# Performance work log

Measured on AMD Instinct MI355X. Metric: run time of the kernel, lower is better.

The kernel has to match this reference:

```python
import jax, jax.numpy as jnp
import numpy as np
import math

B, S, D, H = 4, 1024, 1024, 16
DH = D // H  # 64
NEG = -100000000000.0


def setup_inputs() -> dict:
    key = jax.random.key(0)
    ks = jax.random.split(key, 9)
    sc_in = 1.0 / math.sqrt(D)
    sc_h = 1.0 / math.sqrt(DH)
    return {
        "x": jax.random.normal(ks[0], (B, S, D), dtype=jnp.float32),
        # per-head projection weights stacked over the head axis [H, D, DH]
        "Wq": jax.random.normal(ks[1], (H, D, DH), dtype=jnp.float32) * sc_in,
        "bq": jnp.zeros((H, DH), dtype=jnp.float32),
        "Wk": jax.random.normal(ks[2], (H, D, DH), dtype=jnp.float32) * sc_in,
        "bk": jnp.zeros((H, DH), dtype=jnp.float32),
        "Wv": jax.random.normal(ks[3], (H, D, DH), dtype=jnp.float32) * sc_in,
        "bv": jnp.zeros((H, DH), dtype=jnp.float32),
        # output feed-forward: Dense(D, gelu) applied to the [B,S,DH] head-sum
        "Wf": jax.random.normal(ks[4], (DH, D), dtype=jnp.float32) * sc_h,
        "bf": jnp.zeros((D,), dtype=jnp.float32),
    }


def reference(x, Wq, bq, Wk, bk, Wv, bv, Wf, bf):
    # per-head q,k,v: [B,H,S,DH]
    q = jnp.einsum('bsd,hde->bhse', x, Wq) + bq[None, :, None, :]
    k = jnp.einsum('bsd,hde->bhse', x, Wk) + bk[None, :, None, :]
    v = jnp.einsum('bsd,hde->bhse', x, Wv) + bv[None, :, None, :]
    scale = 1.0 / math.sqrt(DH)
    # causal mask as in source: triu(ones, 1) * -1e11 added to scores
    mask = jnp.triu(jnp.ones((S, S), dtype=jnp.float32), 1) * NEG
    scores = jnp.einsum('bhse,bhte->bhst', q, k) * scale + mask  # [B,H,S,S]
    w = jax.nn.softmax(scores, axis=-1)
    z = jnp.einsum('bhst,bhte->bhse', w, v)  # [B,H,S,DH]
    # faithful to source bug: heads are SUMMED, not concatenated
    summed = jnp.sum(z, axis=1)  # [B,S,DH]
    # ff Dense with exact (erf) gelu, keras tf.nn.gelu default approximate=False
    out = jax.nn.gelu(summed @ Wf + bf, approximate=False)  # [B,S,D]
    # dropout is identity at inference
    return out
```

## Files before the change

### kernel.cpp

```cpp
#include <hip/hip_runtime.h>
#include <hip/hip_bf16.h>
#include <math.h>

#define BB 4
#define SS 1024
#define DD 1024
#define HH 16
#define DH 64

#define GM 4096
#define GN 3072
#define GK 1024

typedef __attribute__((ext_vector_type(4))) float f32x4;
typedef __attribute__((ext_vector_type(8))) short bf16x8;

__device__ __forceinline__ unsigned int pack2bf(float a, float b) {
    __hip_bfloat16 x = __float2bfloat16(a), y = __float2bfloat16(b);
    return (unsigned int)__builtin_bit_cast(unsigned short, x) |
           ((unsigned int)__builtin_bit_cast(unsigned short, y) << 16);
}

__device__ __forceinline__ int swz8(int row) { return (row ^ (row >> 2)) & 7; }

__global__ __launch_bounds__(256) void prep_kernel(
    const float* __restrict__ x, __hip_bfloat16* __restrict__ xb,
    const float* __restrict__ Wq, const float* __restrict__ Wk,
    const float* __restrict__ Wv, __hip_bfloat16* __restrict__ WbT,
    const float* __restrict__ Wf, unsigned short* __restrict__ WfT)
{
    const int id  = blockIdx.x;
    const int tid = threadIdx.x;
    __shared__ float tile[64][65];

    if (id < 4096) {
        int i = (id * 256 + tid) * 4;
        float4 xv = *(const float4*)(x + i);
        xb[i + 0] = __float2bfloat16(xv.x);
        xb[i + 1] = __float2bfloat16(xv.y);
        xb[i + 2] = __float2bfloat16(xv.z);
        xb[i + 3] = __float2bfloat16(xv.w);
    } else if (id < 4864) {
        const int idx = id - 4096;
        const int d0  = (idx & 15) * 64;
        const int zh  = idx >> 4;
        const int z   = zh >> 4;
        const int h   = zh & 15;
        const float* W = (z == 0) ? Wq : (z == 1) ? Wk : Wv;
        const float* src = W + (size_t)h * DD * DH;
        #pragma unroll
        for (int p = 0; p < 16; p++) {
            int d = p * 4 + (tid >> 6);
            int e = tid & 63;
            tile[d][e] = src[(size_t)(d0 + d) * DH + e];
        }
        __syncthreads();
        #pragma unroll
        for (int p = 0; p < 16; p++) {
            int e = p * 4 + (tid >> 6);
            int d = tid & 63;
            WbT[(size_t)(z * 1024 + h * 64 + e) * GK + d0 + d] =
                __float2bfloat16(tile[d][e]);
        }
    } else {
        const int d0 = (id - 4864) * 64;
        #pragma unroll
        for (int p = 0; p < 16; p++) {
            int e  = p * 4 + (tid >> 6);
            int dd = tid & 63;
            tile[e][dd] = Wf[(size_t)e * DD + d0 + dd];
        }
        __syncthreads();
        #pragma unroll
        for (int p = 0; p < 16; p++) {
            int dd = p * 4 + (tid >> 6);
            int e  = tid & 63;
            __hip_bfloat16 hb = __float2bfloat16(tile[e][dd]);
            WfT[(size_t)(d0 + dd) * DH + e] =
                __builtin_bit_cast(unsigned short, hb);
        }
    }
}

__global__ __launch_bounds__(256) void gemm_qkv(
    const unsigned short* __restrict__ A,
    const unsigned short* __restrict__ Bt,
    const float* __restrict__ bq, const float* __restrict__ bk,
    const float* __restrict__ bv,
    unsigned short* __restrict__ q, unsigned short* __restrict__ k,
    unsigned short* __restrict__ v)
{
    __shared__ unsigned short As[2][128 * 32];
    __shared__ unsigned short Bs[2][128 * 32];

    const int tid  = threadIdx.x;
    const int wave = tid >> 6;
    const int lane = tid & 63;
    const int m0 = blockIdx.x * 128;
    const int n0 = blockIdx.y * 128;
    const int wy = wave >> 1, wx = wave & 1;
    const bool vblk = (n0 >= 2048);

    f32x4 acc[4][4];
    #pragma unroll
    for (int i = 0; i < 4; i++)
        #pragma unroll
        for (int j = 0; j < 4; j++)
            acc[i][j] = (f32x4){0.f, 0.f, 0.f, 0.f};

    const int lrow2 = lane >> 2;
    const int lslot = lane & 3;
    const int kchsw = lslot ^ ((lrow2 >> 1) & 3);

    #define STAGE(bufidx, ki)                                                  \
        {                                                                      \
            int k0 = (ki) * 32;                                                \
            _Pragma("unroll")                                                  \
            for (int c = 0; c < 2; c++) {                                      \
                int region = wave * 2 + c;                                     \
                int row = region * 16 + lrow2;                                 \
                const unsigned short* ga =                                     \
                    A + (size_t)(m0 + row) * GK + k0 + kchsw * 8;              \
                const unsigned short* gb =                                     \
                    Bt + (size_t)(n0 + row) * GK + k0 + kchsw * 8;             \
                __builtin_amdgcn_global_load_lds(                              \
                    (const __attribute__((address_space(1))) unsigned int*)ga, \
                    (__attribute__((address_space(3))) unsigned int*)          \
                        (&As[bufidx][region * 512]), 16, 0, 0);                \
                __builtin_amdgcn_global_load_lds(                              \
                    (const __attribute__((address_space(1))) unsigned int*)gb, \
                    (__attribute__((address_space(3))) unsigned int*)          \
                        (&Bs[bufidx][region * 512]), 16, 0, 0);                \
            }                                                                  \
        }

    STAGE(0, 0);

    const int mrow = lane & 15;
    const int quad = lane >> 4;

    for (int ki = 0; ki < 32; ki++) {
        __syncthreads();
        if (ki < 31) STAGE((ki + 1) & 1, ki + 1);

        const unsigned short* uA = &As[ki & 1][0];
        const unsigned short* uB = &Bs[ki & 1][0];

        bf16x8 af[4], bfr[4];
        #pragma unroll
        for (int mt = 0; mt < 4; mt++) {
            int row = wy * 64 + mt * 16 + mrow;
            int chunk = quad ^ ((row >> 1) & 3);
            af[mt] = *(const bf16x8*)(uA + row * 32 + chunk * 8);
        }
        #pragma unroll
        for (int nt = 0; nt < 4; nt++) {
            int row = wx * 64 + nt * 16 + mrow;
            int chunk = quad ^ ((row >> 1) & 3);
            bfr[nt] = *(const bf16x8*)(uB + row * 32 + chunk * 8);
        }
        if (vblk) {
            #pragma unroll
            for (int mt = 0; mt < 4; mt++)
                #pragma unroll
                for (int nt = 0; nt < 4; nt++)
                    acc[mt][nt] = __builtin_amdgcn_mfma_f32_16x16x32_bf16(
                        af[mt], bfr[nt], acc[mt][nt], 0, 0, 0);
        } else {
            #pragma unroll
            for (int nt = 0; nt < 4; nt++)
                #pragma unroll
                for (int mt = 0; mt < 4; mt++)
                    acc[nt][mt] = __builtin_amdgcn_mfma_f32_16x16x32_bf16(
                        bfr[nt], af[mt], acc[nt][mt], 0, 0, 0);
        }
    }
    #undef STAGE

    const int cl = lane & 15;
    const int h  = ((n0 + wx * 64) >> 6) & 15;

    if (!vblk) {
        const int z = n0 >> 10;
        const float* bias = (z == 0) ? bq : bk;
        unsigned short* outp = (z == 0) ? q : k;
        const float sc = (z == 0) ? 0.125f : 1.0f;
        #pragma unroll
        for (int nt = 0; nt < 4; nt++) {
            int ebase = nt * 16 + quad * 4;
            float4 b4 = *(const float4*)(bias + h * 64 + ebase);
            #pragma unroll
            for (int mt = 0; mt < 4; mt++) {
                int m = m0 + wy * 64 + mt * 16 + cl;
                int b = m >> 10, s = m & 1023;
                f32x4 a = acc[nt][mt];
                float v0 = (a[0] + b4.x) * sc;
                float v1 = (a[1] + b4.y) * sc;
                float v2 = (a[2] + b4.z) * sc;
                float v3 = (a[3] + b4.w) * sc;
                uint2 pk = make_uint2(pack2bf(v0, v1), pack2bf(v2, v3));
                *(uint2*)(outp + ((size_t)((b * 16 + h) * 1024 + s)) * 64 + ebase) = pk;
            }
        }
    } else {
        #pragma unroll
        for (int nt = 0; nt < 4; nt++) {
            int e = nt * 16 + cl;
            float bb = bv[h * 64 + e];
            #pragma unroll
            for (int mt = 0; mt < 4; mt++) {
                int rbase = m0 + wy * 64 + mt * 16 + quad * 4;
                int b = rbase >> 10, s = rbase & 1023;
                f32x4 a = acc[mt][nt];
                uint2 pk = make_uint2(pack2bf(a[0] + bb, a[1] + bb),
                                      pack2bf(a[2] + bb, a[3] + bb));
                *(uint2*)(v + ((size_t)((b * 16 + h) * 64 + e)) * 1024 + s) = pk;
            }
        }
    }
}

__global__ __launch_bounds__(256) void flash_attn(
    const unsigned short* __restrict__ qg, const unsigned short* __restrict__ kg,
    const unsigned short* __restrict__ vtg, float* __restrict__ summed)
{
    __shared__ unsigned short Qs[4096];
    __shared__ unsigned short Ks[2][4096];
    __shared__ unsigned short Vts[2][4096];

    const int x  = blockIdx.x;
    const int y  = blockIdx.y;
    const int qi = (x + (y & 15) + ((y >> 4) << 2)) & 15;
    const int q0 = qi * 64;
    const int bh = y;
    const int b  = bh >> 4;
    const int tid  = threadIdx.x;
    const int wave = tid >> 6;
    const int lane = tid & 63;
    const int lrow = lane >> 3;
    const int lcs  = lane & 7;
    const int m16  = lane & 15;
    const int quad = lane >> 4;

    const unsigned short* qb = qg + (size_t)bh * SS * DH;
    const unsigned short* kb = kg + (size_t)bh * SS * DH;
    const unsigned short* vb = vtg + (size_t)bh * SS * DH;

    #pragma unroll
    for (int c = 0; c < 2; c++) {
        int region = wave * 2 + c;
        int row = region * 8 + lrow;
        int g = lcs ^ swz8(row);
        __builtin_amdgcn_global_load_lds(
            (const __attribute__((address_space(1))) unsigned int*)
                (qb + (size_t)(q0 + row) * DH + g * 8),
            (__attribute__((address_space(3))) unsigned int*)(Qs + region * 512),
            16, 0, 0);
        __builtin_amdgcn_global_load_lds(
            (const __attribute__((address_space(1))) unsigned int*)
                (kb + (size_t)row * DH + g * 8),
            (__attribute__((address_space(3))) unsigned int*)(&Ks[0][region * 512]),
            16, 0, 0);
        __builtin_amdgcn_global_load_lds(
            (const __attribute__((address_space(1))) unsigned int*)
                (vb + (size_t)row * SS + g * 8),
            (__attribute__((address_space(3))) unsigned int*)(&Vts[0][region * 512]),
            16, 0, 0);
    }

    f32x4 accO[4];
    float lsum = 0.f;
    #pragma unroll
    for (int nt = 0; nt < 4; nt++) accO[nt] = (f32x4){0.f, 0.f, 0.f, 0.f};

    bf16x8 af0, af1;
    const int rloc = wave * 16 + m16;

    for (int tt = 0; tt <= qi; tt++) {
        __syncthreads();

        if (tt == 0) {
            int row = wave * 16 + m16;
            af0 = *(const bf16x8*)(Qs + row * 64 + ((quad ^ swz8(row)) * 8));
            af1 = *(const bf16x8*)(Qs + row * 64 + (((4 + quad) ^ swz8(row)) * 8));
        }

        if (tt < qi) {
            const int t1 = (tt + 1) * 64;
            const int bn = (tt + 1) & 1;
            #pragma unroll
            for (int c = 0; c < 2; c++) {
                int region = wave * 2 + c;
                int row = region * 8 + lrow;
                int g = lcs ^ swz8(row);
                __builtin_amdgcn_global_load_lds(
                    (const __attribute__((address_space(1))) unsigned int*)
                        (kb + (size_t)(t1 + row) * DH + g * 8),
                    (__attribute__((address_space(3))) unsigned int*)
                        (&Ks[bn][region * 512]), 16, 0, 0);
                __builtin_amdgcn_global_load_lds(
                    (const __attribute__((address_space(1))) unsigned int*)
                        (vb + (size_t)row * SS + t1 + g * 8),
                    (__attribute__((address_space(3))) unsigned int*)
                        (&Vts[bn][region * 512]), 16, 0, 0);
            }
        }

        const unsigned short* uK = &Ks[tt & 1][0];
        const unsigned short* uV = &Vts[tt & 1][0];

        f32x4 acc[4];
        #pragma unroll
        for (int nt = 0; nt < 4; nt++) {
            int row = ((nt & 2) << 4) + ((m16 >> 2) << 3) + ((nt & 1) << 2) + (m16 & 3);
            bf16x8 kf0 = *(const bf16x8*)(uK + row * 64 + ((quad ^ swz8(row)) * 8));
            bf16x8 kf1 = *(const bf16x8*)(uK + row * 64 + (((4 + quad) ^ swz8(row)) * 8));
            f32x4 a = (f32x4){0.f, 0.f, 0.f, 0.f};
            a = __builtin_amdgcn_mfma_f32_16x16x32_bf16(kf0, af0, a, 0, 0, 0);
            a = __builtin_amdgcn_mfma_f32_16x16x32_bf16(kf1, af1, a, 0, 0, 0);
            acc[nt] = a;
        }

        const bool diag = (tt == qi);
        bf16x8 pf0, pf1;
        #pragma unroll
        for (int nt = 0; nt < 4; nt++) {
            #pragma unroll
            for (int r = 0; r < 4; r++) {
                int tl = ((nt & 2) << 4) + (quad << 3) + ((nt & 1) << 2) + r;
                float s = acc[nt][r];
                if (diag && tl > rloc) s = -1e30f;
                float p = __expf(s);
                lsum += p;
                __hip_bfloat16 hb = __float2bfloat16(p);
                short pb = (short)__builtin_bit_cast(unsigned short, hb);
                int j = ((nt & 1) << 2) + r;
                if (nt < 2) pf0[j] = pb; else pf1[j] = pb;
            }
        }

        #pragma unroll
        for (int nt = 0; nt < 4; nt++) {
            int row = nt * 16 + m16;
            bf16x8 vf0 = *(const bf16x8*)(uV + row * 64 + ((quad ^ swz8(row)) * 8));
            bf16x8 vf1 = *(const bf16x8*)(uV + row * 64 + (((4 + quad) ^ swz8(row)) * 8));
            accO[nt] = __builtin_amdgcn_mfma_f32_16x16x32_bf16(vf0, pf0, accO[nt],
                                                               0, 0, 0);
            accO[nt] = __builtin_amdgcn_mfma_f32_16x16x32_bf16(vf1, pf1, accO[nt],
                                                               0, 0, 0);
        }
    }

    float l = lsum;
    l += __shfl_xor(l, 16);
    l += __shfl_xor(l, 32);
    const float invl = 1.f / l;

    __syncthreads();
    float* buf = (wave < 2) ? (float*)&Ks[0][0] : (float*)&Vts[0][0];
    buf += (wave & 1) * (16 * 66);
    #pragma unroll
    for (int nt = 0; nt < 4; nt++) {
        f32x4 w4 = accO[nt];
        w4 *= invl;
        *(f32x4*)(buf + m16 * 66 + nt * 16 + quad * 4) = w4;
    }
    __asm__ volatile("s_waitcnt lgkmcnt(0)" ::: "memory");

    float* dstbase = summed + ((size_t)b * SS + q0 + wave * 16) * DH;
    #pragma unroll
    for (int rr = 0; rr < 16; rr++) {
        float valr = buf[rr * 66 + lane];
        atomicAdd(dstbase + (size_t)rr * DH + lane, valr);
    }
}

__global__ __launch_bounds__(256) void ff_mfma(
    const float* __restrict__ summed, const unsigned short* __restrict__ WfT,
    const float* __restrict__ bfb, float* __restrict__ out)
{
    __shared__ unsigned short As[128 * 64];
    __shared__ unsigned short Bs[128 * 64];

    const int tid  = threadIdx.x;
    const int wave = tid >> 6;
    const int lane = tid & 63;
    const int m0 = blockIdx.x * 128;
    const int n0 = blockIdx.y * 128;
    const int wy = wave >> 1, wx = wave & 1;
    const int lrow = lane >> 3;
    const int lcs  = lane & 7;

    #pragma unroll
    for (int c = 0; c < 4; c++) {
        int row = (wave * 4 + c) * 8 + lrow;
        int chunk = lcs ^ (row & 7);
        __builtin_amdgcn_global_load_lds(
            (const __attribute__((address_space(1))) unsigned int*)
                (WfT + (size_t)(n0 + row) * DH + chunk * 8),
            (__attribute__((address_space(3))) unsigned int*)
                (Bs + ((wave * 4 + c) * 64) * 8), 16, 0, 0);
    }
    #pragma unroll
    for (int i = 0; i < 4; i++) {
        int chunkid = tid + i * 256;
        int row = chunkid >> 3, c = chunkid & 7;
        const float* src = summed + (size_t)(m0 + row) * DH + c * 8;
        float4 a = *(const float4*)src;
        float4 bq = *(const float4*)(src + 4);
        uint4 pk;
        pk.x = pack2bf(a.x, a.y);  pk.y = pack2bf(a.z, a.w);
        pk.z = pack2bf(bq.x, bq.y); pk.w = pack2bf(bq.z, bq.w);
        *(uint4*)(As + row * 64 + ((c ^ (row & 7)) * 8)) = pk;
    }
    __syncthreads();

    f32x4 acc[4][4];
    #pragma unroll
    for (int i = 0; i < 4; i++)
        #pragma unroll
        for (int j = 0; j < 4; j++)
            acc[i][j] = (f32x4){0.f, 0.f, 0.f, 0.f};

    const int mrow = lane & 15;
    const int quad = lane >> 4;
    #pragma unroll
    for (int ks = 0; ks < 2; ks++) {
        bf16x8 af[4], bfr[4];
        #pragma unroll
        for (int mt = 0; mt < 4; mt++) {
            int row = wy * 64 + mt * 16 + mrow;
            int chunk = (ks * 4 + quad) ^ (row & 7);
            af[mt] = *(const bf16x8*)(As + row * 64 + chunk * 8);
        }
        #pragma unroll
        for (int nt = 0; nt < 4; nt++) {
            int row = wx * 64 + nt * 16 + mrow;
            int chunk = (ks * 4 + quad) ^ (row & 7);
            bfr[nt] = *(const bf16x8*)(Bs + row * 64 + chunk * 8);
        }
        #pragma unroll
        for (int mt = 0; mt < 4; mt++)
            #pragma unroll
            for (int nt = 0; nt < 4; nt++)
                acc[mt][nt] = __builtin_amdgcn_mfma_f32_16x16x32_bf16(
                    af[mt], bfr[nt], acc[mt][nt], 0, 0, 0);
    }

    const int cl = lane & 15;
    #pragma unroll
    for (int nt = 0; nt < 4; nt++) {
        int d = n0 + wx * 64 + nt * 16 + cl;
        float bb = bfb[d];
        #pragma unroll
        for (int mt = 0; mt < 4; mt++) {
            int rbase = m0 + wy * 64 + mt * 16 + quad * 4;
            #pragma unroll
            for (int r = 0; r < 4; r++) {
                float vA = acc[mt][nt][r] + bb;
                out[(size_t)(rbase + r) * DD + d] =
                    0.5f * vA * (1.f + erff(vA * 0.70710678118654752f));
            }
        }
    }
}

extern "C" void kernel_launch(void* const* d_in, const int* in_sizes, int n_in,
                              void* d_out, int out_size, void* d_ws, size_t ws_size,
                              hipStream_t stream) {
    const float* x  = (const float*)d_in[0];
    const float* Wq = (const float*)d_in[1];
    const float* bq = (const float*)d_in[2];
    const float* Wk = (const float*)d_in[3];
    const float* bk = (const float*)d_in[4];
    const float* Wv = (const float*)d_in[5];
    const float* bv = (const float*)d_in[6];
    const float* Wf = (const float*)d_in[7];
    const float* bf = (const float*)d_in[8];
    float* out = (float*)d_out;

    const size_t per = (size_t)BB * HH * SS * DH;
    unsigned short* q   = (unsigned short*)d_ws;
    unsigned short* k   = q + per;
    unsigned short* v   = k + per;
    float* summed       = (float*)(v + per);
    __hip_bfloat16* xb  = (__hip_bfloat16*)(summed + (size_t)BB * SS * DH);
    __hip_bfloat16* WbT = xb + (size_t)BB * SS * DD;
    unsigned short* WfT = (unsigned short*)(WbT + (size_t)GN * GK);

    hipMemsetAsync(summed, 0, (size_t)BB * SS * DH * sizeof(float), stream);

    prep_kernel<<<4880, 256, 0, stream>>>(x, (__hip_bfloat16*)xb,
                                          Wq, Wk, Wv, (__hip_bfloat16*)WbT,
                                          Wf, WfT);

    gemm_qkv<<<dim3(GM / 128, GN / 128), 256, 0, stream>>>(
        (const unsigned short*)xb, (const unsigned short*)WbT,
        bq, bk, bv, q, k, v);

    flash_attn<<<dim3(SS / 64, BB * HH), 256, 0, stream>>>(q, k, v, summed);

    ff_mfma<<<dim3(GM / 128, DD / 128), 256, 0, stream>>>(summed, WfT, bf, out);
}
```

Baseline: 182.5 us.

## Load QKV GEMM B operand directly to registers and deepen K tile to 64

The QKV projection GEMM now stages only the activation tile A through LDS, with a 64-wide K slice and XOR swizzling. Each wave loads its weight fragments for B straight from global memory into registers and prefetches the next K step one iteration ahead. The grid is also swapped so consecutive blocks walk along N and share the same A rows. The aim is to halve LDS traffic, cut barrier count and improve cache reuse, at the cost of more registers and B loads that go uncoalesced and unshared across waves.

```diff
diff --git a/kernel.cpp b/kernel.cpp
--- a/kernel.cpp
+++ b/kernel.cpp
@@ -90,17 +90,21 @@
     unsigned short* __restrict__ q, unsigned short* __restrict__ k,
     unsigned short* __restrict__ v)
 {
-    __shared__ unsigned short As[2][128 * 32];
-    __shared__ unsigned short Bs[2][128 * 32];
+    __shared__ unsigned short As[2][128 * 64];
 
     const int tid  = threadIdx.x;
     const int wave = tid >> 6;
     const int lane = tid & 63;
-    const int m0 = blockIdx.x * 128;
-    const int n0 = blockIdx.y * 128;
+    const int n0 = blockIdx.x * 128;
+    const int m0 = blockIdx.y * 128;
     const int wy = wave >> 1, wx = wave & 1;
     const bool vblk = (n0 >= 2048);
 
+    const int lrow = lane >> 3;
+    const int lcs  = lane & 7;
+    const int mrow = lane & 15;
+    const int quad = lane >> 4;
+
     f32x4 acc[4][4];
     #pragma unroll
     for (int i = 0; i < 4; i++)
@@ -108,74 +112,80 @@
         for (int j = 0; j < 4; j++)
             acc[i][j] = (f32x4){0.f, 0.f, 0.f, 0.f};
 
-    const int lrow2 = lane >> 2;
-    const int lslot = lane & 3;
-    const int kchsw = lslot ^ ((lrow2 >> 1) & 3);
-
-    #define STAGE(bufidx, ki)                                                  \
+    #define STAGE_A(bufidx, ko)                                                \
         {                                                                      \
-            int k0 = (ki) * 32;                                                \
             _Pragma("unroll")                                                  \
-            for (int c = 0; c < 2; c++) {                                      \
-                int region = wave * 2 + c;                                     \
-                int row = region * 16 + lrow2;                                 \
-                const unsigned short* ga =                                     \
-                    A + (size_t)(m0 + row) * GK + k0 + kchsw * 8;              \
-                const unsigned short* gb =                                     \
-                    Bt + (size_t)(n0 + row) * GK + k0 + kchsw * 8;             \
+            for (int c = 0; c < 4; c++) {                                      \
+                int region = wave * 4 + c;                                     \
+                int row = region * 8 + lrow;                                   \
+                int chunk = lcs ^ (row & 7);                                   \
                 __builtin_amdgcn_global_load_lds(                              \
-                    (const __attribute__((address_space(1))) unsigned int*)ga, \
+                    (const __attribute__((address_space(1))) unsigned int*)    \
+                        (A + (size_t)(m0 + row) * GK + (ko) + chunk * 8),      \
                     (__attribute__((address_space(3))) unsigned int*)          \
                         (&As[bufidx][region * 512]), 16, 0, 0);                \
-                __builtin_amdgcn_global_load_lds(                              \
-                    (const __attribute__((address_space(1))) unsigned int*)gb, \
-                    (__attribute__((address_space(3))) unsigned int*)          \
-                        (&Bs[bufidx][region * 512]), 16, 0, 0);                \
             }                                                                  \
         }
 
-    STAGE(0, 0);
-
-    const int mrow = lane & 15;
-    const int quad = lane >> 4;
-
-    for (int ki = 0; ki < 32; ki++) {
+    const unsigned short* colbase =
+        Bt + (size_t)(n0 + wx * 64 + mrow) * GK + quad * 8;
+
+    STAGE_A(0, 0);
+
+    bf16x8 bnxt[8];
+    #pragma unroll
+    for (int ks = 0; ks < 2; ks++)
+        #pragma unroll
+        for (int nt = 0; nt < 4; nt++)
+            bnxt[ks * 4 + nt] =
+                *(const bf16x8*)(colbase + nt * 16 * GK + ks * 32);
+
+    for (int ki = 0; ki < 16; ki++) {
         __syncthreads();
-        if (ki < 31) STAGE((ki + 1) & 1, ki + 1);
-
-        const unsigned short* uA = &As[ki & 1][0];
-        const unsigned short* uB = &Bs[ki & 1][0];
-
-        bf16x8 af[4], bfr[4];
-        #pragma unroll
-        for (int mt = 0; mt < 4; mt++) {
-            int row = wy * 64 + mt * 16 + mrow;
-            int chunk = quad ^ ((row >> 1) & 3);
-            af[mt] = *(const bf16x8*)(uA + row * 32 + chunk * 8);
-        }
-        #pragma unroll
-        for (int nt = 0; nt < 4; nt++) {
-            int row = wx * 64 + nt * 16 + mrow;
-            int chunk = quad ^ ((row >> 1) & 3);
-            bfr[nt] = *(const bf16x8*)(uB + row * 32 + chunk * 8);
-        }
-        if (vblk) {
-            #pragma unroll
-            for (int mt = 0; mt < 4; mt++)
+        if (ki < 15) STAGE_A((ki + 1) & 1, (ki + 1) * 64);
+
+        bf16x8 bcur[8];
+        #pragma unroll
+        for (int j = 0; j < 8; j++) bcur[j] = bnxt[j];
+
+        if (ki < 15) {
+            const int ko = (ki + 1) * 64;
+            #pragma unroll
+            for (int ks = 0; ks < 2; ks++)
                 #pragma unroll
                 for (int nt = 0; nt < 4; nt++)
-                    acc[mt][nt] = __builtin_amdgcn_mfma_f32_16x16x32_bf16(
-                        af[mt], bfr[nt], acc[mt][nt], 0, 0, 0);
-        } else {
-            #pragma unroll
-            for (int nt = 0; nt < 4; nt++)
+                    bnxt[ks * 4 + nt] =
+                        *(const bf16x8*)(colbase + nt * 16 * GK + ko + ks * 32);
+        }
+
+        const unsigned short* uA = &As[ki & 1][0];
+        #pragma unroll
+        for (int ks = 0; ks < 2; ks++) {
+            bf16x8 af[4];
+            #pragma unroll
+            for (int mt = 0; mt < 4; mt++) {
+                int row = wy * 64 + mt * 16 + mrow;
+                int chunk = (ks * 4 + quad) ^ (row & 7);
+                af[mt] = *(const bf16x8*)(uA + row * 64 + chunk * 8);
+            }
+            if (vblk) {
                 #pragma unroll
                 for (int mt = 0; mt < 4; mt++)
-                    acc[nt][mt] = __builtin_amdgcn_mfma_f32_16x16x32_bf16(
-                        bfr[nt], af[mt], acc[nt][mt], 0, 0, 0);
-        }
-    }
-    #undef STAGE
+                    #pragma unroll
+                    for (int nt = 0; nt < 4; nt++)
+                        acc[mt][nt] = __builtin_amdgcn_mfma_f32_16x16x32_bf16(
+                            af[mt], bcur[ks * 4 + nt], acc[mt][nt], 0, 0, 0);
+            } else {
+                #pragma unroll
+                for (int nt = 0; nt < 4; nt++)
+                    #pragma unroll
+                    for (int mt = 0; mt < 4; mt++)
+                        acc[nt][mt] = __builtin_amdgcn_mfma_f32_16x16x32_bf16(
+                            bcur[ks * 4 + nt], af[mt], acc[nt][mt], 0, 0, 0);
+            }
+        }
+    }
+    #undef STAGE_A
 
     const int cl = lane & 15;
     const int h  = ((n0 + wx * 64) >> 6) & 15;
@@ -494,7 +504,7 @@
                                           Wq, Wk, Wv, (__hip_bfloat16*)WbT,
                                           Wf, WfT);
 
-    gemm_qkv<<<dim3(GM / 128, GN / 128), 256, 0, stream>>>(
+    gemm_qkv<<<dim3(GN / 128, GM / 128), 256, 0, stream>>>(
         (const unsigned short*)xb, (const unsigned short*)WbT,
         bq, bk, bv, q, k, v);
 
```

After: 192.8 us. 5.6% more time.
